# Performance work log

Measured on AMD Instinct MI355X. Metric: run time of the kernel, lower is better.

The kernel has to match this reference:

```python
import jax, jax.numpy as jnp
import numpy as np
import math

NUM_HEADS = 16
NUM_KV_HEADS = 4
HEAD_DIM = 128


def rotate_half(x):
    x1, x2 = x[..., : x.shape[-1] // 2], x[..., x.shape[-1] // 2 :]
    return jnp.concatenate((-x2, x1), axis=-1)


def setup_inputs() -> dict:
    key = jax.random.key(0)
    ks = jax.random.split(key, 7)
    B, L, D = 2, 2048, 2048
    hidden_states = jax.random.normal(ks[0], (B, L, D), dtype=jnp.float32)
    # realistic RoPE tables
    inv_freq = 1.0 / (10000.0 ** (np.arange(0, HEAD_DIM, 2, dtype=np.float32) / HEAD_DIM))
    t = np.arange(L, dtype=np.float32)
    freqs = np.outer(t, inv_freq)
    emb = np.concatenate([freqs, freqs], axis=-1)
    cos = jnp.asarray(np.cos(emb), dtype=jnp.float32)
    sin = jnp.asarray(np.sin(emb), dtype=jnp.float32)
    s = 1.0 / math.sqrt(D)
    Wq = jax.random.normal(ks[1], (D, NUM_HEADS * HEAD_DIM), dtype=jnp.float32) * s
    Wk = jax.random.normal(ks[2], (D, NUM_KV_HEADS * HEAD_DIM), dtype=jnp.float32) * s
    Wv = jax.random.normal(ks[3], (D, NUM_KV_HEADS * HEAD_DIM), dtype=jnp.float32) * s
    Wo = jax.random.normal(ks[4], (NUM_HEADS * HEAD_DIM, D), dtype=jnp.float32) * s
    return {"hidden_states": hidden_states, "cos": cos, "sin": sin,
            "Wq": Wq, "Wk": Wk, "Wv": Wv, "Wo": Wo}


def reference(hidden_states, cos, sin, Wq, Wk, Wv, Wo):
    B, L, D = hidden_states.shape
    H, KVH, Dh = NUM_HEADS, NUM_KV_HEADS, HEAD_DIM
    q = (hidden_states @ Wq).reshape(B, L, H, Dh)
    k = (hidden_states @ Wk).reshape(B, L, KVH, Dh)
    v = (hidden_states @ Wv).reshape(B, L, KVH, Dh)
    # RoPE: cos/sin are [L, Dh] broadcast over batch and heads
    c = cos[None, :, None, :]
    s = sin[None, :, None, :]
    q = q * c + rotate_half(q) * s
    k = k * c + rotate_half(k) * s
    # GQA: repeat kv heads to match query heads
    rep = H // KVH
    k = jnp.repeat(k, rep, axis=2)
    v = jnp.repeat(v, rep, axis=2)
    scale = 1.0 / math.sqrt(Dh)
    # [B, H, L, L]
    attn = jnp.einsum('bqhd,bkhd->bhqk', q, k) * scale
    i = jnp.arange(L)[:, None]
    j = jnp.arange(L)[None, :]
    attn = jnp.where(i >= j, attn, -jnp.inf)
    attn = jax.nn.softmax(attn, axis=-1)
    out = jnp.einsum('bhqk,bkhd->bqhd', attn, v).reshape(B, L, H * Dh)
    return out @ Wo
```

## Files before the change

kernel.cpp:

```cpp
#include <hip/hip_runtime.h>
#include <hip/hip_bf16.h>

typedef __attribute__((ext_vector_type(8))) short bf16x8;
typedef __attribute__((ext_vector_type(4))) float f32x4;
typedef __attribute__((ext_vector_type(4))) short short4v;

__device__ __forceinline__ unsigned short f2bf(float f) {
  union { float f; unsigned u; } x; x.f = f;
  return (unsigned short)((x.u + 0x7FFFu + ((x.u >> 16) & 1u)) >> 16);
}

__device__ __forceinline__ short f2bf_hw(float f) {
  __hip_bfloat16 h = __float2bfloat16(f);
  return *(short*)&h;
}

__device__ __forceinline__ void lds_cp16(const void* g, void* l) {
  __builtin_amdgcn_global_load_lds(
      (const __attribute__((address_space(1))) void*)g,
      (__attribute__((address_space(3))) void*)l,
      16, 0, 0);
}

#define GBAR() do { __builtin_amdgcn_s_barrier(); __builtin_amdgcn_sched_barrier(0); } while (0)

__global__ __launch_bounds__(256) void cast_x(const float* __restrict__ in,
                                              short* __restrict__ out, int n4) {
  int i = blockIdx.x * 256 + threadIdx.x;
  if (i >= n4) return;
  float4 v = reinterpret_cast<const float4*>(in)[i];
  short4v o;
  o.x = (short)f2bf(v.x); o.y = (short)f2bf(v.y);
  o.z = (short)f2bf(v.z); o.w = (short)f2bf(v.w);
  reinterpret_cast<short4v*>(out)[i] = o;
}

__global__ __launch_bounds__(256) void transp_cast(const float* __restrict__ in,
                                                   short* __restrict__ out,
                                                   int K, int N) {
  __shared__ float t[32][33];
  int bn = blockIdx.x * 32, bk = blockIdx.y * 32;
  int tx = threadIdx.x, ty = threadIdx.y;
  for (int i = ty; i < 32; i += 8)
    t[i][tx] = in[(size_t)(bk + i) * N + bn + tx];
  __syncthreads();
  for (int i = ty; i < 32; i += 8)
    out[(size_t)(bn + i) * K + bk + tx] = (short)f2bf(t[tx][i]);
}

__global__ __launch_bounds__(256) void transp_v(const short* __restrict__ V,
                                                short* __restrict__ VTo) {
  __shared__ short t[32][34];
  const int hd = blockIdx.z;
  const int p0 = blockIdx.x * 32, d0 = blockIdx.y * 32;
  const short* src = V + (size_t)hd * 2048 * 128;
  short* dst = VTo + (size_t)hd * 2048 * 128;
  int tx = threadIdx.x, ty = threadIdx.y;
  for (int i = ty; i < 32; i += 8)
    t[i][tx] = src[(size_t)(p0 + i) * 128 + d0 + tx];
  __syncthreads();
  for (int i = ty; i < 32; i += 8)
    dst[(size_t)(d0 + i) * 2048 + p0 + tx] = t[tx][i];
}

template <int BM, int EPI>
__global__ __launch_bounds__(512, 2) void gemm8p(
    const short* __restrict__ A, const short* __restrict__ Bt,
    float* __restrict__ C,
    short* __restrict__ Qo, short* __restrict__ Ko, short* __restrict__ Vo,
    const float* __restrict__ cosT, const float* __restrict__ sinT,
    int N, int Kd, int nbm) {
  constexpr int NM = BM / 64;
  __shared__ __align__(16) short As[2][BM * 64];
  __shared__ __align__(16) short Bs[2][256 * 64];
  const int tid = threadIdx.x;
  const int l = tid & 63, l15 = l & 15, l4 = l >> 4;
  const int wid = tid >> 6, wr = wid >> 1, wc = wid & 1;
  const int cpx = gridDim.x >> 3;
  const int sid = (blockIdx.x & 7) * cpx + (blockIdx.x >> 3);
  const int bm = sid % nbm, bn = sid / nbm;

  const int srow = tid >> 3;
  const int sch = tid & 7;

  auto stA = [&](int dbuf, int k0, int i) {
    const int rl = srow + i * 64;
    const int c = sch ^ (rl & 7);
    lds_cp16(A + (size_t)(bm * BM + rl) * Kd + k0 + c * 8,
             (char*)As[dbuf] + tid * 16 + i * 8192);
  };
  auto stB = [&](int dbuf, int k0, int j) {
    const int rl = srow + j * 64;
    const int c = sch ^ (rl & 7);
    lds_cp16(Bt + (size_t)(bn * 256 + rl) * Kd + k0 + c * 8,
             (char*)Bs[dbuf] + tid * 16 + j * 8192);
  };
  auto rdA = [&](int dbuf, int m, int kb) {
    const int row = wr * (BM / 4) + m * 16 + l15;
    return *(const bf16x8*)((const char*)As[dbuf] + (row << 7) +
                            ((kb * 64 + l4 * 16) ^ ((row & 7) << 4)));
  };
  auto rdB = [&](int dbuf, int nh, int f, int kb) {
    const int row = wc * 128 + nh * 64 + f * 16 + l15;
    return *(const bf16x8*)((const char*)Bs[dbuf] + (row << 7) +
                            ((kb * 64 + l4 * 16) ^ ((row & 7) << 4)));
  };

  f32x4 acc[NM][8];
#pragma unroll
  for (int m = 0; m < NM; m++)
#pragma unroll
    for (int n = 0; n < 8; n++) acc[m][n] = (f32x4){0.f, 0.f, 0.f, 0.f};

  const int NT = Kd >> 6;

#pragma unroll
  for (int i = 0; i < NM; i++) stA(0, 0, i);
#pragma unroll
  for (int j = 0; j < 4; j++) stB(0, 0, j);
  asm volatile("s_waitcnt vmcnt(0)" ::: "memory");
  GBAR();

  for (int kt = 0; kt < NT; kt++) {
    const int buf = kt & 1, nbf = buf ^ 1;
    const bool stg = (kt + 1 < NT);
    const int k1 = (kt + 1) << 6;
    bf16x8 a[NM], b[4];

#pragma unroll
    for (int m = 0; m < NM; m++) a[m] = rdA(buf, m, 0);
#pragma unroll
    for (int f = 0; f < 4; f++) b[f] = rdB(buf, 0, f, 0);
    if (stg) { stA(nbf, k1, 0); stA(nbf, k1, 1); }
    if (stg) asm volatile("s_waitcnt vmcnt(2)" ::: "memory");
    else     asm volatile("s_waitcnt vmcnt(0)" ::: "memory");
    GBAR();
    asm volatile("s_waitcnt lgkmcnt(0)" ::: "memory");
    __builtin_amdgcn_sched_barrier(0);
    __builtin_amdgcn_s_setprio(1);
#pragma unroll
    for (int m = 0; m < NM; m++)
#pragma unroll
      for (int f = 0; f < 4; f++)
        acc[m][f] = __builtin_amdgcn_mfma_f32_16x16x32_bf16(a[m], b[f], acc[m][f], 0, 0, 0);
    __builtin_amdgcn_s_setprio(0);
    GBAR();

#pragma unroll
    for (int f = 0; f < 4; f++) b[f] = rdB(buf, 1, f, 0);
    if (stg) {
      if (BM == 256) { stA(nbf, k1, 2); stA(nbf, k1, 3); }
      else           { stB(nbf, k1, 0); stB(nbf, k1, 2); }
    }
    GBAR();
    asm volatile("s_waitcnt lgkmcnt(0)" ::: "memory");
    __builtin_amdgcn_sched_barrier(0);
    __builtin_amdgcn_s_setprio(1);
#pragma unroll
    for (int m = 0; m < NM; m++)
#pragma unroll
      for (int f = 0; f < 4; f++)
        acc[m][4 + f] = __builtin_amdgcn_mfma_f32_16x16x32_bf16(a[m], b[f], acc[m][4 + f], 0, 0, 0);
    __builtin_amdgcn_s_setprio(0);
    GBAR();

#pragma unroll
    for (int m = 0; m < NM; m++) a[m] = rdA(buf, m, 1);
#pragma unroll
    for (int f = 0; f < 4; f++) b[f] = rdB(buf, 0, f, 1);
    if (stg) {
      if (BM == 256) { stB(nbf, k1, 0); stB(nbf, k1, 2); }
      else           { stB(nbf, k1, 1); stB(nbf, k1, 3); }
    }
    GBAR();
    asm volatile("s_waitcnt lgkmcnt(0)" ::: "memory");
    __builtin_amdgcn_sched_barrier(0);
    __builtin_amdgcn_s_setprio(1);
#pragma unroll
    for (int m = 0; m < NM; m++)
#pragma unroll
      for (int f = 0; f < 4; f++)
        acc[m][f] = __builtin_amdgcn_mfma_f32_16x16x32_bf16(a[m], b[f], acc[m][f], 0, 0, 0);
    __builtin_amdgcn_s_setprio(0);
    GBAR();

#pragma unroll
    for (int f = 0; f < 4; f++) b[f] = rdB(buf, 1, f, 1);
    if (stg && BM == 256) { stB(nbf, k1, 1); stB(nbf, k1, 3); }
    if (stg) asm volatile("s_waitcnt vmcnt(2)" ::: "memory");
    GBAR();
    asm volatile("s_waitcnt lgkmcnt(0)" ::: "memory");
    __builtin_amdgcn_sched_barrier(0);
    __builtin_amdgcn_s_setprio(1);
#pragma unroll
    for (int m = 0; m < NM; m++)
#pragma unroll
      for (int f = 0; f < 4; f++)
        acc[m][4 + f] = __builtin_amdgcn_mfma_f32_16x16x32_bf16(a[m], b[f], acc[m][4 + f], 0, 0, 0);
    __builtin_amdgcn_s_setprio(0);
    GBAR();
  }

  if (EPI == 0) {
#pragma unroll
    for (int m = 0; m < NM; m++) {
      const int grow = bm * BM + wr * (BM / 4) + m * 16 + l4 * 4;
#pragma unroll
      for (int ni = 0; ni < 8; ni++) {
        const int col = bn * 256 + wc * 128 + (ni >> 2) * 64 + (ni & 3) * 16 + l15;
#pragma unroll
        for (int r = 0; r < 4; r++)
          C[(size_t)(grow + r) * N + col] = acc[m][ni][r];
      }
    }
  } else {
    const int head = bn * 2 + wc;
#pragma unroll
    for (int m = 0; m < NM; m++) {
#pragma unroll
      for (int r = 0; r < 4; r++) {
        const int grow = bm * BM + wr * (BM / 4) + m * 16 + l4 * 4 + r;
        const int bb = grow >> 11, pos = grow & 2047;
        if (head < 20) {
          float c4[4], s4[4];
#pragma unroll
          for (int ni = 0; ni < 4; ni++) {
            const int dh = ni * 16 + l15;
            c4[ni] = cosT[pos * 128 + dh];
            s4[ni] = sinT[pos * 128 + dh];
          }
          short* dst;
          if (head < 16) dst = Qo + ((size_t)(bb * 16 + head) * 2048 + pos) * 128;
          else           dst = Ko + ((size_t)(bb * 4 + (head - 16)) * 2048 + pos) * 128;
#pragma unroll
          for (int ni = 0; ni < 4; ni++) {
            const int dh = ni * 16 + l15;
            float xlo = acc[m][ni][r], xhi = acc[m][ni + 4][r];
            dst[dh]      = (short)f2bf(xlo * c4[ni] - xhi * s4[ni]);
            dst[dh + 64] = (short)f2bf(xhi * c4[ni] + xlo * s4[ni]);
          }
        } else {
          short* dst = Vo + ((size_t)(bb * 4 + (head - 20)) * 2048 + pos) * 128;
#pragma unroll
          for (int ni = 0; ni < 8; ni++)
            dst[(ni >> 2) * 64 + (ni & 3) * 16 + l15] = (short)f2bf(acc[m][ni][r]);
        }
      }
    }
  }
}

__global__ __launch_bounds__(256) void attn_fwd(
    const short* __restrict__ Q, const short* __restrict__ K,
    const short* __restrict__ VT, short* __restrict__ AO) {
  __shared__ __align__(16) short Ks[2][64 * 128];
  __shared__ __align__(16) short VTs[2][128 * 64];
  __shared__ __align__(16) short Pl[4][16 * 64];
  const int tid = threadIdx.x;
  const int w = tid >> 6, l = tid & 63;
  const int l15 = l & 15, l4 = l >> 4;
  const int bid = blockIdx.x;
  const int lg = (bid & 7) * 64 + (bid >> 3);
  const int bh = lg >> 4, pp = lg & 15;
  const int b = bh >> 4, h = bh & 15, kv = h >> 2;
  const short* Qbase = Q + (size_t)(b * 16 + h) * 2048 * 128;
  const short* Kbase = K + (size_t)(b * 4 + kv) * 2048 * 128;
  const short* VTb   = VT + (size_t)(b * 4 + kv) * 2048 * 128;

  int rk[4], ck[4], dv[4], kc[4];
#pragma unroll
  for (int i = 0; i < 4; i++) {
    const int c = tid + i * 256;
    rk[i] = c >> 4; ck[i] = (c & 15) ^ (rk[i] & 7);
    dv[i] = c >> 3; kc[i] = (c & 7) ^ (dv[i] & 7);
  }

  const float SCL = 0.08838834764831845f * 1.4426950408889634f;

  bf16x8 ones;
#pragma unroll
  for (int j = 0; j < 8; j++) ones[j] = (short)0x3F80;

  for (int qq = 0; qq < 2; qq++) {
    const int qt = qq ? (31 - pp) : pp;
    const int q0w = qt * 64 + w * 16;

    bf16x8 qf[4];
#pragma unroll
    for (int kb = 0; kb < 4; kb++)
      qf[kb] = *(const bf16x8*)(Qbase + (size_t)(q0w + l15) * 128 + kb * 32 + l4 * 8);

    f32x4 oacc[8];
#pragma unroll
    for (int i = 0; i < 8; i++) oacc[i] = (f32x4){0.f, 0.f, 0.f, 0.f};
    f32x4 lacc = (f32x4){0.f, 0.f, 0.f, 0.f};

    const int ntiles = qt + 1;

    __syncthreads();
#pragma unroll
    for (int i = 0; i < 4; i++) {
      lds_cp16(Kbase + (size_t)rk[i] * 128 + ck[i] * 8, (char*)Ks[0] + i * 4096 + tid * 16);
      lds_cp16(VTb + (size_t)dv[i] * 2048 + kc[i] * 8,  (char*)VTs[0] + i * 4096 + tid * 16);
    }

    for (int nt = 0; nt < ntiles; nt++) {
      const int k0 = nt * 64, buf = nt & 1;
      __syncthreads();
      if (nt + 1 < ntiles) {
        const int kn = k0 + 64, bnx = buf ^ 1;
#pragma unroll
        for (int i = 0; i < 4; i++) {
          lds_cp16(Kbase + (size_t)(kn + rk[i]) * 128 + ck[i] * 8,
                   (char*)Ks[bnx] + i * 4096 + tid * 16);
          lds_cp16(VTb + (size_t)dv[i] * 2048 + kn + kc[i] * 8,
                   (char*)VTs[bnx] + i * 4096 + tid * 16);
        }
      }

      f32x4 sa[4];
#pragma unroll
      for (int kg = 0; kg < 4; kg++) sa[kg] = (f32x4){0.f, 0.f, 0.f, 0.f};
      __builtin_amdgcn_s_setprio(1);
#pragma unroll
      for (int kg = 0; kg < 4; kg++) {
        const int row = kg * 16 + l15;
        const int swz = (row & 7) << 4;
#pragma unroll
        for (int kb = 0; kb < 4; kb++) {
          const char* kp = (const char*)Ks[buf] + row * 256 + ((kb * 64 + l4 * 16) ^ swz);
          sa[kg] = __builtin_amdgcn_mfma_f32_16x16x32_bf16(qf[kb], *(const bf16x8*)kp, sa[kg], 0, 0, 0);
        }
      }
      __builtin_amdgcn_s_setprio(0);

      float p[4][4];
      const bool domask = (k0 + 63 > q0w);
#pragma unroll
      for (int kg = 0; kg < 4; kg++)
#pragma unroll
        for (int r = 0; r < 4; r++) {
          float pv = exp2f(sa[kg][r] * SCL);
          if (domask) {
            int qrow = q0w + l4 * 4 + r;
            if (k0 + kg * 16 + l15 > qrow) pv = 0.f;
          }
          p[kg][r] = pv;
        }

#pragma unroll
      for (int r = 0; r < 4; r++) {
        const int rw = l4 * 4 + r;
        const int swz = (rw & 7) << 4;
#pragma unroll
        for (int kg = 0; kg < 4; kg++)
          *(short*)((char*)Pl[w] + (rw * 128 + ((kg * 32 + l15 * 2) ^ swz))) =
              f2bf_hw(p[kg][r]);
      }
      asm volatile("s_waitcnt lgkmcnt(0)" ::: "memory");
      bf16x8 pf[2];
#pragma unroll
      for (int ks = 0; ks < 2; ks++)
        pf[ks] = *(const bf16x8*)((const char*)Pl[w] +
                 (l15 * 128 + ((ks * 64 + l4 * 16) ^ ((l15 & 7) << 4))));

      __builtin_amdgcn_s_setprio(1);
#pragma unroll
      for (int nb = 0; nb < 8; nb++) {
        const int d = nb * 16 + l15;
        const int dsw = (d & 7) << 4;
#pragma unroll
        for (int ks = 0; ks < 2; ks++) {
          const char* vp = (const char*)VTs[buf] + d * 128 + ((ks * 64 + l4 * 16) ^ dsw);
          oacc[nb] = __builtin_amdgcn_mfma_f32_16x16x32_bf16(pf[ks], *(const bf16x8*)vp, oacc[nb], 0, 0, 0);
        }
      }
      lacc = __builtin_amdgcn_mfma_f32_16x16x32_bf16(pf[0], ones, lacc, 0, 0, 0);
      lacc = __builtin_amdgcn_mfma_f32_16x16x32_bf16(pf[1], ones, lacc, 0, 0, 0);
      __builtin_amdgcn_s_setprio(0);
    }

#pragma unroll
    for (int r = 0; r < 4; r++) {
      float inv = 1.0f / lacc[r];
      size_t rowb = ((size_t)b * 2048 + q0w + l4 * 4 + r) * 2048 + h * 128;
#pragma unroll
      for (int nb = 0; nb < 8; nb++)
        AO[rowb + nb * 16 + l15] = f2bf_hw(oacc[nb][r] * inv);
    }
  }
}

extern "C" void kernel_launch(void* const* d_in, const int* in_sizes, int n_in,
                              void* d_out, int out_size, void* d_ws, size_t ws_size,
                              hipStream_t stream) {
  const float* hs   = (const float*)d_in[0];
  const float* cosT = (const float*)d_in[1];
  const float* sinT = (const float*)d_in[2];
  const float* Wq   = (const float*)d_in[3];
  const float* Wk   = (const float*)d_in[4];
  const float* Wv   = (const float*)d_in[5];
  const float* Wo   = (const float*)d_in[6];
  float* out = (float*)d_out;

  char* p = (char*)d_ws;
  short* Xb   = (short*)p; p += (size_t)4096 * 2048 * 2;
  short* Wqkv = (short*)p; p += (size_t)3072 * 2048 * 2;
  short* Wot  = (short*)p; p += (size_t)2048 * 2048 * 2;
  short* Qb   = (short*)p; p += (size_t)2 * 16 * 2048 * 128 * 2;
  short* Kb   = (short*)p; p += (size_t)2 * 4 * 2048 * 128 * 2;
  short* Vb   = (short*)p; p += (size_t)2 * 4 * 2048 * 128 * 2;
  short* VTb  = (short*)p; p += (size_t)2 * 4 * 2048 * 128 * 2;
  short* AO   = Xb;

  cast_x<<<8192, 256, 0, stream>>>(hs, Xb, 2097152);
  transp_cast<<<dim3(64, 64), dim3(32, 8), 0, stream>>>(Wq, Wqkv, 2048, 2048);
  transp_cast<<<dim3(16, 64), dim3(32, 8), 0, stream>>>(Wk, Wqkv + (size_t)2048 * 2048, 2048, 512);
  transp_cast<<<dim3(16, 64), dim3(32, 8), 0, stream>>>(Wv, Wqkv + (size_t)2560 * 2048, 2048, 512);
  transp_cast<<<dim3(64, 64), dim3(32, 8), 0, stream>>>(Wo, Wot, 2048, 2048);

  gemm8p<256, 1><<<192, 512, 0, stream>>>(Xb, Wqkv, nullptr, Qb, Kb, Vb,
                                          cosT, sinT, 3072, 2048, 16);
  transp_v<<<dim3(64, 4, 8), dim3(32, 8), 0, stream>>>(Vb, VTb);
  attn_fwd<<<512, 256, 0, stream>>>(Qb, Kb, VTb, AO);
  gemm8p<128, 0><<<256, 512, 0, stream>>>(AO, Wot, out, nullptr, nullptr, nullptr,
                                          nullptr, nullptr, 2048, 2048, 32);
}
```

Measured before the change: 220.8 us.

## Switch attention to 32x32x16 MFMA with 2 waves and register-shuffled P

Measured after the change: 248.0 us. 12.3% more time.

```diff
diff --git a/kernel.cpp b/kernel.cpp
--- a/kernel.cpp
+++ b/kernel.cpp
@@ -3,7 +3,9 @@
 
 typedef __attribute__((ext_vector_type(8))) short bf16x8;
 typedef __attribute__((ext_vector_type(4))) float f32x4;
+typedef __attribute__((ext_vector_type(16))) float f32x16;
 typedef __attribute__((ext_vector_type(4))) short short4v;
+typedef __attribute__((ext_vector_type(4))) unsigned u32x4;
 
 __device__ __forceinline__ unsigned short f2bf(float f) {
   union { float f; unsigned u; } x; x.f = f;
@@ -13,6 +15,12 @@
 __device__ __forceinline__ short f2bf_hw(float f) {
   __hip_bfloat16 h = __float2bfloat16(f);
   return *(short*)&h;
+}
+
+__device__ __forceinline__ unsigned pk2(float a, float b) {
+  float2 t2; t2.x = a; t2.y = b;
+  __hip_bfloat162 t = __float22bfloat162_rn(t2);
+  return *(unsigned*)&t;
 }
 
 __device__ __forceinline__ void lds_cp16(const void* g, void* l) {
@@ -250,15 +258,14 @@
   }
 }
 
-__global__ __launch_bounds__(256) void attn_fwd(
+__global__ __launch_bounds__(128) void attn_fwd(
     const short* __restrict__ Q, const short* __restrict__ K,
     const short* __restrict__ VT, short* __restrict__ AO) {
   __shared__ __align__(16) short Ks[2][64 * 128];
   __shared__ __align__(16) short VTs[2][128 * 64];
-  __shared__ __align__(16) short Pl[4][16 * 64];
   const int tid = threadIdx.x;
   const int w = tid >> 6, l = tid & 63;
-  const int l15 = l & 15, l4 = l >> 4;
+  const int l31 = l & 31, hi = l >> 5;
   const int bid = blockIdx.x;
   const int lg = (bid & 7) * 64 + (bid >> 3);
   const int bh = lg >> 4, pp = lg & 15;
@@ -267,41 +274,46 @@
   const short* Kbase = K + (size_t)(b * 4 + kv) * 2048 * 128;
   const short* VTb   = VT + (size_t)(b * 4 + kv) * 2048 * 128;
 
-  int rk[4], ck[4], dv[4], kc[4];
-#pragma unroll
-  for (int i = 0; i < 4; i++) {
-    const int c = tid + i * 256;
-    rk[i] = c >> 4; ck[i] = (c & 15) ^ (rk[i] & 7);
-    dv[i] = c >> 3; kc[i] = (c & 7) ^ (dv[i] & 7);
+  int koff[8], voff[8];
+#pragma unroll
+  for (int i = 0; i < 8; i++) {
+    const int c = tid + i * 128;
+    const int rk = c >> 4, ck = (c & 15) ^ (rk & 7);
+    const int dv = c >> 3, kc = (c & 7) ^ (dv & 7);
+    koff[i] = rk * 128 + ck * 8;
+    voff[i] = dv * 2048 + kc * 8;
   }
 
   const float SCL = 0.08838834764831845f * 1.4426950408889634f;
-
   bf16x8 ones;
 #pragma unroll
   for (int j = 0; j < 8; j++) ones[j] = (short)0x3F80;
 
   for (int qq = 0; qq < 2; qq++) {
     const int qt = qq ? (31 - pp) : pp;
-    const int q0w = qt * 64 + w * 16;
-
-    bf16x8 qf[4];
-#pragma unroll
-    for (int kb = 0; kb < 4; kb++)
-      qf[kb] = *(const bf16x8*)(Qbase + (size_t)(q0w + l15) * 128 + kb * 32 + l4 * 8);
-
-    f32x4 oacc[8];
-#pragma unroll
-    for (int i = 0; i < 8; i++) oacc[i] = (f32x4){0.f, 0.f, 0.f, 0.f};
-    f32x4 lacc = (f32x4){0.f, 0.f, 0.f, 0.f};
+    const int q0w = qt * 64 + w * 32;
+
+    bf16x8 qf[8];
+#pragma unroll
+    for (int kb = 0; kb < 8; kb++)
+      qf[kb] = *(const bf16x8*)(Qbase + (size_t)(q0w + l31) * 128 + kb * 16 + hi * 8);
+
+    f32x16 oacc[4];
+#pragma unroll
+    for (int nb = 0; nb < 4; nb++)
+#pragma unroll
+      for (int r = 0; r < 16; r++) oacc[nb][r] = 0.f;
+    f32x16 lacc;
+#pragma unroll
+    for (int r = 0; r < 16; r++) lacc[r] = 0.f;
 
     const int ntiles = qt + 1;
 
     __syncthreads();
 #pragma unroll
-    for (int i = 0; i < 4; i++) {
-      lds_cp16(Kbase + (size_t)rk[i] * 128 + ck[i] * 8, (char*)Ks[0] + i * 4096 + tid * 16);
-      lds_cp16(VTb + (size_t)dv[i] * 2048 + kc[i] * 8,  (char*)VTs[0] + i * 4096 + tid * 16);
+    for (int i = 0; i < 8; i++) {
+      lds_cp16(Kbase + koff[i], (char*)Ks[0] + i * 2048 + tid * 16);
+      lds_cp16(VTb + voff[i],   (char*)VTs[0] + i * 2048 + tid * 16);
     }
 
     for (int nt = 0; nt < ntiles; nt++) {
@@ -310,83 +322,86 @@
       if (nt + 1 < ntiles) {
         const int kn = k0 + 64, bnx = buf ^ 1;
 #pragma unroll
-        for (int i = 0; i < 4; i++) {
-          lds_cp16(Kbase + (size_t)(kn + rk[i]) * 128 + ck[i] * 8,
-                   (char*)Ks[bnx] + i * 4096 + tid * 16);
-          lds_cp16(VTb + (size_t)dv[i] * 2048 + kn + kc[i] * 8,
-                   (char*)VTs[bnx] + i * 4096 + tid * 16);
+        for (int i = 0; i < 8; i++) {
+          lds_cp16(Kbase + (size_t)kn * 128 + koff[i], (char*)Ks[bnx] + i * 2048 + tid * 16);
+          lds_cp16(VTb + kn + voff[i],                 (char*)VTs[bnx] + i * 2048 + tid * 16);
         }
       }
 
-      f32x4 sa[4];
-#pragma unroll
-      for (int kg = 0; kg < 4; kg++) sa[kg] = (f32x4){0.f, 0.f, 0.f, 0.f};
+      f32x16 sa[2];
+#pragma unroll
+      for (int r = 0; r < 16; r++) { sa[0][r] = 0.f; sa[1][r] = 0.f; }
       __builtin_amdgcn_s_setprio(1);
 #pragma unroll
-      for (int kg = 0; kg < 4; kg++) {
-        const int row = kg * 16 + l15;
+      for (int kg = 0; kg < 2; kg++) {
+        const int row = kg * 32 + l31;
         const int swz = (row & 7) << 4;
 #pragma unroll
-        for (int kb = 0; kb < 4; kb++) {
-          const char* kp = (const char*)Ks[buf] + row * 256 + ((kb * 64 + l4 * 16) ^ swz);
-          sa[kg] = __builtin_amdgcn_mfma_f32_16x16x32_bf16(qf[kb], *(const bf16x8*)kp, sa[kg], 0, 0, 0);
+        for (int kb = 0; kb < 8; kb++) {
+          const char* kp = (const char*)Ks[buf] + row * 256 + ((kb * 32 + hi * 16) ^ swz);
+          sa[kg] = __builtin_amdgcn_mfma_f32_32x32x16_bf16(*(const bf16x8*)kp, qf[kb], sa[kg], 0, 0, 0);
         }
       }
       __builtin_amdgcn_s_setprio(0);
 
-      float p[4][4];
       const bool domask = (k0 + 63 > q0w);
-#pragma unroll
-      for (int kg = 0; kg < 4; kg++)
-#pragma unroll
-        for (int r = 0; r < 4; r++) {
+      const int qrow = q0w + l31;
+#pragma unroll
+      for (int kg = 0; kg < 2; kg++)
+#pragma unroll
+        for (int r = 0; r < 16; r++) {
           float pv = exp2f(sa[kg][r] * SCL);
           if (domask) {
-            int qrow = q0w + l4 * 4 + r;
-            if (k0 + kg * 16 + l15 > qrow) pv = 0.f;
+            const int key = k0 + kg * 32 + (r & 3) + 8 * (r >> 2) + 4 * hi;
+            if (key > qrow) pv = 0.f;
           }
-          p[kg][r] = pv;
+          sa[kg][r] = pv;
         }
 
-#pragma unroll
-      for (int r = 0; r < 4; r++) {
-        const int rw = l4 * 4 + r;
-        const int swz = (rw & 7) << 4;
-#pragma unroll
-        for (int kg = 0; kg < 4; kg++)
-          *(short*)((char*)Pl[w] + (rw * 128 + ((kg * 32 + l15 * 2) ^ swz))) =
-              f2bf_hw(p[kg][r]);
-      }
-      asm volatile("s_waitcnt lgkmcnt(0)" ::: "memory");
-      bf16x8 pf[2];
-#pragma unroll
-      for (int ks = 0; ks < 2; ks++)
-        pf[ks] = *(const bf16x8*)((const char*)Pl[w] +
-                 (l15 * 128 + ((ks * 64 + l4 * 16) ^ ((l15 & 7) << 4))));
+      bf16x8 pa[4];
+#pragma unroll
+      for (int ks = 0; ks < 4; ks++) {
+        const int kg = ks >> 1, r0 = (ks & 1) * 8;
+        unsigned X = pk2(sa[kg][r0 + 0], sa[kg][r0 + 1]);
+        unsigned Y = pk2(sa[kg][r0 + 2], sa[kg][r0 + 3]);
+        unsigned Z = pk2(sa[kg][r0 + 4], sa[kg][r0 + 5]);
+        unsigned W = pk2(sa[kg][r0 + 6], sa[kg][r0 + 7]);
+        unsigned s0 = hi ? X : Z, s1 = hi ? Y : W;
+        unsigned g0 = (unsigned)__shfl((int)s0, l ^ 32);
+        unsigned g1 = (unsigned)__shfl((int)s1, l ^ 32);
+        u32x4 pw;
+        pw.x = hi ? g0 : X;
+        pw.y = hi ? g1 : Y;
+        pw.z = hi ? Z : g0;
+        pw.w = hi ? W : g1;
+        pa[ks] = *(bf16x8*)&pw;
+      }
 
       __builtin_amdgcn_s_setprio(1);
 #pragma unroll
-      for (int nb = 0; nb < 8; nb++) {
-        const int d = nb * 16 + l15;
-        const int dsw = (d & 7) << 4;
-#pragma unroll
-        for (int ks = 0; ks < 2; ks++) {
-          const char* vp = (const char*)VTs[buf] + d * 128 + ((ks * 64 + l4 * 16) ^ dsw);
-          oacc[nb] = __builtin_amdgcn_mfma_f32_16x16x32_bf16(pf[ks], *(const bf16x8*)vp, oacc[nb], 0, 0, 0);
+      for (int nb = 0; nb < 4; nb++) {
+        const int row = nb * 32 + l31;
+        const int swz = (row & 7) << 4;
+#pragma unroll
+        for (int ks = 0; ks < 4; ks++) {
+          const char* vp = (const char*)VTs[buf] + row * 128 + ((ks * 32 + hi * 16) ^ swz);
+          oacc[nb] = __builtin_amdgcn_mfma_f32_32x32x16_bf16(pa[ks], *(const bf16x8*)vp, oacc[nb], 0, 0, 0);
         }
       }
-      lacc = __builtin_amdgcn_mfma_f32_16x16x32_bf16(pf[0], ones, lacc, 0, 0, 0);
-      lacc = __builtin_amdgcn_mfma_f32_16x16x32_bf16(pf[1], ones, lacc, 0, 0, 0);
+#pragma unroll
+      for (int ks = 0; ks < 4; ks++)
+        lacc = __builtin_amdgcn_mfma_f32_32x32x16_bf16(pa[ks], ones, lacc, 0, 0, 0);
       __builtin_amdgcn_s_setprio(0);
     }
 
 #pragma unroll
-    for (int r = 0; r < 4; r++) {
-      float inv = 1.0f / lacc[r];
-      size_t rowb = ((size_t)b * 2048 + q0w + l4 * 4 + r) * 2048 + h * 128;
-#pragma unroll
-      for (int nb = 0; nb < 8; nb++)
-        AO[rowb + nb * 16 + l15] = f2bf_hw(oacc[nb][r] * inv);
+    for (int r = 0; r < 16; r++) {
+      const float inv = 1.0f / lacc[r];
+      const int q = q0w + (r & 3) + 8 * (r >> 2) + 4 * hi;
+      const size_t rowb = ((size_t)b * 2048 + q) * 2048 + h * 128;
+#pragma unroll
+      for (int nb = 0; nb < 4; nb++)
+        AO[rowb + nb * 32 + l31] = f2bf_hw(oacc[nb][r] * inv);
     }
   }
 }
@@ -422,7 +437,7 @@
   gemm8p<256, 1><<<192, 512, 0, stream>>>(Xb, Wqkv, nullptr, Qb, Kb, Vb,
                                           cosT, sinT, 3072, 2048, 16);
   transp_v<<<dim3(64, 4, 8), dim3(32, 8), 0, stream>>>(Vb, VTb);
-  attn_fwd<<<512, 256, 0, stream>>>(Qb, Kb, VTb, AO);
+  attn_fwd<<<512, 128, 0, stream>>>(Qb, Kb, VTb, AO);
   gemm8p<128, 0><<<256, 512, 0, stream>>>(AO, Wot, out, nullptr, nullptr, nullptr,
                                           nullptr, nullptr, 2048, 2048, 32);
 }
```
